# Kernel tuning notes

Hardware: AMD Instinct MI355X
Metric: run time of the kernel (lower is better)

The kernel has to match this reference:

```python
import jax, jax.numpy as jnp
import numpy as np

B, C, H, W = 8, 192, 56, 56
OUT, K = 192, 9
BN_EPS = 1e-5


def _l2_normalize(x, axis):
    # matches torch F.normalize: x / max(||x||, eps)
    n = jnp.sqrt(jnp.sum(x * x, axis=axis, keepdims=True))
    return x / jnp.maximum(n, 1e-12)


def _knn_idx(x_bnc, k):
    # dense pairwise squared distances, then k nearest (includes self)
    sq = jnp.sum(x_bnc * x_bnc, axis=-1, keepdims=True)            # (b,n,1)
    dist = sq - 2.0 * jnp.einsum('bnc,bmc->bnm', x_bnc, x_bnc) + jnp.swapaxes(sq, 1, 2)
    _, idx = jax.lax.top_k(-dist, k)                                # (b,n,k)
    return idx


def setup_inputs() -> dict:
    key = jax.random.key(0)
    k1, k2 = jax.random.split(key)
    fan_in = 2 * C
    return {
        'x': jax.random.normal(k1, (B, C, H, W), dtype=jnp.float32),
        'conv_w': jax.random.normal(k2, (OUT, 2 * C), dtype=jnp.float32) * np.sqrt(2.0 / fan_in),
        'conv_b': jnp.zeros((OUT,), dtype=jnp.float32),
        'bn_gamma': jnp.ones((OUT,), dtype=jnp.float32),
        'bn_beta': jnp.zeros((OUT,), dtype=jnp.float32),
    }


def reference(x, conv_w, conv_b, bn_gamma, bn_beta):
    b, c, h, w = x.shape
    n = h * w
    xf = x.reshape(b, c, n)                      # (b,c,n) node features
    xt = jnp.swapaxes(xf, 1, 2)                  # (b,n,c)

    # graph build on L2-normalized features (torch does this under no_grad)
    xn = _l2_normalize(xt, axis=-1)
    idx = _knn_idx(jax.lax.stop_gradient(xn), K)  # (b,n,K) neighbor ids

    # gather neighbors; center gather is identity (center_idx == arange)
    x_j = jnp.take_along_axis(xt[:, :, None, :], idx[..., None], axis=1)  # (b,n,K,c)
    x_i = xt[:, :, None, :]                                               # (b,n,1,c)
    feat = jnp.concatenate([jnp.broadcast_to(x_i, x_j.shape), x_j - x_i], axis=-1)  # (b,n,K,2c)

    # 1x1 conv == per-edge linear
    y = jnp.einsum('bnke,oe->bnko', feat, conv_w) + conv_b                # (b,n,K,out)

    # BatchNorm2d (training-mode batch stats over b,n,K per channel)
    mean = jnp.mean(y, axis=(0, 1, 2))
    var = jnp.var(y, axis=(0, 1, 2))
    y = (y - mean) * jax.lax.rsqrt(var + BN_EPS) * bn_gamma + bn_beta

    y = jax.nn.gelu(y, approximate=False)
    y = jnp.max(y, axis=2)                        # max over K neighbors -> (b,n,out)
    return jnp.transpose(y, (0, 2, 1)).reshape(b, -1, h, w)
```

## Files before the change

### kernel.cpp

```cpp
#include <hip/hip_runtime.h>
#include <hip/hip_bf16.h>
#include <math.h>

#define BB 8
#define CC 192
#define HH 56
#define WW 56
#define NPTS 3136
#define OUTC 192
#define KNN 9
#define NTILES 49
#define NCH 2
#define NT4 98
#define NBLK4 (NT4 * BB)

typedef __bf16 bf16x8 __attribute__((ext_vector_type(8)));
typedef float  f32x16 __attribute__((ext_vector_type(16)));
typedef int    i32x4  __attribute__((ext_vector_type(4)));

__device__ __forceinline__ unsigned short f2bf(float f) {
    unsigned u = __float_as_uint(f);
    u += 0x7fffu + ((u >> 16) & 1u);
    return (unsigned short)(u >> 16);
}
__device__ __forceinline__ float bf2f(unsigned short h) {
    return __uint_as_float(((unsigned)h) << 16);
}
__device__ __forceinline__ float gelu_f(float z) {
    return 0.5f * z * (1.0f + erff(z * 0.70710678118654752f));
}

__device__ __forceinline__ void ins12u32(unsigned (&t)[12], unsigned key) {
    if (key >= t[11]) return;
    t[11] = key;
#pragma unroll
    for (int q = 11; q > 0; --q) {
        const unsigned a = t[q-1], bq = t[q];
        const bool sw = bq < a;
        t[q-1] = sw ? bq : a;
        t[q]   = sw ? a : bq;
    }
}

__device__ __forceinline__ void ins12u(unsigned long long (&t)[12], unsigned long long key) {
    if (key >= t[11]) return;
    t[11] = key;
#pragma unroll
    for (int q = 11; q > 0; --q) {
        const unsigned long long a = t[q-1], bq = t[q];
        const bool sw = bq < a;
        t[q-1] = sw ? bq : a;
        t[q]   = sw ? a : bq;
    }
}

__device__ __forceinline__ void ins9f(float (&d)[9], int (&ix)[9], float nd, int ni) {
    if (!((nd < d[8]) || (nd == d[8] && ni < ix[8]))) return;
    d[8] = nd; ix[8] = ni;
#pragma unroll
    for (int q = 8; q > 0; --q) {
        if ((d[q] < d[q-1]) || (d[q] == d[q-1] && ix[q] < ix[q-1])) {
            float t = d[q]; d[q] = d[q-1]; d[q-1] = t;
            int t2 = ix[q]; ix[q] = ix[q-1]; ix[q-1] = t2;
        }
    }
}

__global__ __launch_bounds__(256) void k1_normalize(const float* __restrict__ x,
                                                    float* __restrict__ xn,
                                                    unsigned short* __restrict__ xh,
                                                    unsigned short* __restrict__ xl,
                                                    float* __restrict__ normv,
                                                    float* __restrict__ sqv) {
    const int b  = blockIdx.y;
    const int n0 = blockIdx.x * 64;
    __shared__ float tile[64 * 193];
    __shared__ float red[4][64];
    __shared__ float inv[64];
    const int tid = threadIdx.x;
    const int p   = tid & 63;
    const int cg  = tid >> 6;
    const float* xb = x + (size_t)b * CC * NPTS;

    float acc = 0.f;
#pragma unroll 4
    for (int t = 0; t < 48; ++t) {
        const int c = cg * 48 + t;
        const float v = xb[(size_t)c * NPTS + n0 + p];
        tile[p * 193 + c] = v;
        acc += v * v;
    }
    red[cg][p] = acc;
    __syncthreads();
    if (cg == 0) {
        const float s  = red[0][p] + red[1][p] + red[2][p] + red[3][p];
        float nc = sqrtf(s);
        nc = fmaxf(nc, 1e-12f);
        normv[b * NPTS + n0 + p] = nc;
        const float iv = 1.0f / nc;
        inv[p] = iv;
        sqv[b * NPTS + n0 + p] = s * iv * iv;
    }
    __syncthreads();
    const size_t base = ((size_t)b * NPTS + n0) * CC;
    float* dst = xn + base;
    for (int q = tid; q < 64 * CC / 4; q += 256) {
        const int f   = q * 4;
        const int row = f / CC;
        const int c   = f - row * CC;
        const float iv = inv[row];
        float4 v;
        v.x = tile[row * 193 + c + 0] * iv;
        v.y = tile[row * 193 + c + 1] * iv;
        v.z = tile[row * 193 + c + 2] * iv;
        v.w = tile[row * 193 + c + 3] * iv;
        *(float4*)&dst[f] = v;
        ushort4 hv, lv;
        hv.x = f2bf(v.x); lv.x = f2bf(v.x - bf2f(hv.x));
        hv.y = f2bf(v.y); lv.y = f2bf(v.y - bf2f(hv.y));
        hv.z = f2bf(v.z); lv.z = f2bf(v.z - bf2f(hv.z));
        hv.w = f2bf(v.w); lv.w = f2bf(v.w - bf2f(hv.w));
        *(ushort4*)&xh[base + f] = hv;
        *(ushort4*)&xl[base + f] = lv;
    }
}

__global__ __launch_bounds__(256, 3) void k2_knn(const unsigned short* __restrict__ xh,
                                                 const unsigned short* __restrict__ xl,
                                                 unsigned long long* __restrict__ pd) {
    const int b     = blockIdx.x;
    const int chunk = blockIdx.y;
    const int r0    = blockIdx.z * 64;
    const int t0    = chunk ? 25 : 0;
    const int t1    = chunk ? 49 : 25;

    __shared__ __align__(16) char smem[51200];
    unsigned short* Cs  = (unsigned short*)smem;
    unsigned short* Rk1 = (unsigned short*)(smem + 25600);
    unsigned long long* cdu = (unsigned long long*)smem;

    const int tid  = threadIdx.x;
    const int w    = tid >> 6;
    const int lane = tid & 63;
    const int wc   = w & 1;
    const int wr   = w >> 1;
    const int l31  = lane & 31;
    const int lhi  = lane >> 5;
    const int koffe = lhi * 8;
    const int myrow = wc * 32 + l31;

    const int spnt = tid >> 2;
    const int sj   = tid & 3;

    const size_t rbase = ((size_t)b * NPTS + (r0 + myrow)) * CC;
    bf16x8 Rh0[6], Rl0[6];
#pragma unroll
    for (int c = 0; c < 6; ++c) {
        Rh0[c] = *(const bf16x8*)(const void*)(xh + rbase + c * 16 + koffe);
        Rl0[c] = *(const bf16x8*)(const void*)(xl + rbase + c * 16 + koffe);
    }

    {
        const size_t pb = ((size_t)b * NPTS + r0 + spnt) * CC + 96;
#pragma unroll
        for (int rep = 0; rep < 3; ++rep) {
            const int j = sj + rep * 4;
            *(uint4*)(void*)&Rk1[spnt * 200 + j * 8] =
                *(const uint4*)(const void*)(xh + pb + j * 8);
        }
#pragma unroll
        for (int rep = 0; rep < 3; ++rep) {
            const int j = sj + rep * 4;
            *(uint4*)(void*)&Rk1[spnt * 200 + 96 + j * 8] =
                *(const uint4*)(const void*)(xl + pb + j * 8);
        }
    }

    unsigned t12[12];
#pragma unroll
    for (int q = 0; q < 12; ++q) t12[q] = 0xFFFFFFFFu;

    const int cfb = (wr * 32 + l31) * 200 + koffe;
    const int rlb = myrow * 200 + koffe;

    for (int ct = t0; ct < t1; ++ct) {
        const int c0 = ct * 64;
        __syncthreads();
        {
            const size_t pb = ((size_t)b * NPTS + c0 + spnt) * CC;
#pragma unroll
            for (int rep = 0; rep < 6; ++rep) {
                const int j = sj + rep * 4;
                *(uint4*)(void*)&Cs[spnt * 200 + j * 8] =
                    *(const uint4*)(const void*)(xh + pb + j * 8);
            }
        }
        __syncthreads();

        f32x16 acc;
#pragma unroll
        for (int r = 0; r < 16; ++r) acc[r] = 0.f;

#pragma unroll
        for (int c = 0; c < 6; ++c) {
            const bf16x8 cf = *(const bf16x8*)(const void*)&Cs[cfb + c * 16];
            acc = __builtin_amdgcn_mfma_f32_32x32x16_bf16(cf, Rh0[c], acc, 0, 0, 0);
            acc = __builtin_amdgcn_mfma_f32_32x32x16_bf16(cf, Rl0[c], acc, 0, 0, 0);
        }
#pragma unroll
        for (int c = 0; c < 6; ++c) {
            const bf16x8 cf = *(const bf16x8*)(const void*)&Cs[cfb + (6 + c) * 16];
            const i32x4 th = *(const volatile i32x4*)(const volatile void*)&Rk1[rlb + c * 16];
            const i32x4 tl = *(const volatile i32x4*)(const volatile void*)&Rk1[rlb + 96 + c * 16];
            acc = __builtin_amdgcn_mfma_f32_32x32x16_bf16(cf, __builtin_bit_cast(bf16x8, th), acc, 0, 0, 0);
            acc = __builtin_amdgcn_mfma_f32_32x32x16_bf16(cf, __builtin_bit_cast(bf16x8, tl), acc, 0, 0, 0);
        }
        __syncthreads();
        {
            const size_t pb = ((size_t)b * NPTS + c0 + spnt) * CC;
#pragma unroll
            for (int rep = 0; rep < 6; ++rep) {
                const int j = sj + rep * 4;
                *(uint4*)(void*)&Cs[spnt * 200 + j * 8] =
                    *(const uint4*)(const void*)(xl + pb + j * 8);
            }
        }
        __syncthreads();
#pragma unroll
        for (int c = 0; c < 6; ++c) {
            const bf16x8 cl = *(const bf16x8*)(const void*)&Cs[cfb + c * 16];
            acc = __builtin_amdgcn_mfma_f32_32x32x16_bf16(cl, Rh0[c], acc, 0, 0, 0);
        }
#pragma unroll
        for (int c = 0; c < 6; ++c) {
            const bf16x8 cl = *(const bf16x8*)(const void*)&Cs[cfb + (6 + c) * 16];
            const i32x4 th = *(const volatile i32x4*)(const volatile void*)&Rk1[rlb + c * 16];
            acc = __builtin_amdgcn_mfma_f32_32x32x16_bf16(cl, __builtin_bit_cast(bf16x8, th), acc, 0, 0, 0);
        }

        const unsigned tbase = (unsigned)((ct - t0) << 4);
#pragma unroll
        for (int reg = 0; reg < 16; ++reg) {
            const float d = fmaxf(1.0f - acc[reg], 0.0f);
            const unsigned key = (__float_as_uint(d) & 0xFFFFFE00u) | (tbase | (unsigned)reg);
            ins12u32(t12, key);
        }
    }

    __syncthreads();
#pragma unroll
    for (int q = 0; q < 12; ++q) {
        const unsigned key = t12[q];
        const int tag = (int)(key & 511u);
        const int reg = tag & 15;
        const int col = (t0 + (tag >> 4)) * 64 + wr * 32 + ((reg & 3) + 8 * (reg >> 2) + 4 * lhi);
        cdu[(((wr * 2 + lhi) * 64) + myrow) * 12 + q] = ((unsigned long long)key << 32) | (unsigned)col;
    }
    __syncthreads();
    if (tid < 64) {
        unsigned long long t[12];
#pragma unroll
        for (int q = 0; q < 12; ++q) t[q] = cdu[tid * 12 + q];
        for (int s = 1; s < 4; ++s)
#pragma unroll
            for (int q = 0; q < 12; ++q) ins12u(t, cdu[(s * 64 + tid) * 12 + q]);
        const size_t gbase = ((size_t)b * NPTS + r0 + tid) * (NCH * 12) + chunk * 12;
#pragma unroll
        for (int q = 0; q < 12; ++q) pd[gbase + q] = t[q];
    }
}

__global__ __launch_bounds__(128) void k2b_merge(const float* __restrict__ xn,
                                                 const float* __restrict__ sqv,
                                                 const unsigned long long* __restrict__ pd,
                                                 int* __restrict__ idxout) {
    const int b  = blockIdx.x;
    const int r0 = blockIdx.y * 32;
    __shared__ __align__(16) float xr_s[32][196];
    __shared__ int   ci[32][12];
    __shared__ float dd[32][13];
    __shared__ int   need[32];
    const int tid = threadIdx.x;
    const float* xb = xn + (size_t)b * NPTS * CC;

    for (int q = tid; q < 32 * 48; q += 128) {
        const int row = q / 48, c4 = q - row * 48;
        *(float4*)&xr_s[row][c4 * 4] = *(const float4*)&xb[(size_t)(r0 + row) * CC + c4 * 4];
    }
    if (tid < 32) {
        const size_t base = ((size_t)b * NPTS + r0 + tid) * (NCH * 12);
        unsigned long long t[12];
#pragma unroll
        for (int q = 0; q < 12; ++q) t[q] = pd[base + q];
        for (int s = 1; s < NCH; ++s)
#pragma unroll
            for (int q = 0; q < 12; ++q) ins12u(t, pd[base + s * 12 + q]);
#pragma unroll
        for (int q = 0; q < 12; ++q) ci[tid][q] = (int)(t[q] & 0xFFFFFFFFull);
        const float d9  = __uint_as_float((unsigned)(t[8] >> 32) & 0xFFFFFE00u);
        const float d10 = __uint_as_float((unsigned)(t[9] >> 32) & 0xFFFFFE00u);
        need[tid] = (d10 - d9) < 3e-4f ? 1 : 0;
    }
    __syncthreads();
    {
        const int p = tid >> 2;
        const int s = tid & 3;
        if (need[p]) {
            const float sqn = sqv[(size_t)b * NPTS + r0 + p];
#pragma unroll
            for (int t3 = 0; t3 < 3; ++t3) {
                const int cs2 = s + t3 * 4;
                const int m   = ci[p][cs2];
                const float* xm = xb + (size_t)m * CC;
                float4 a4 = make_float4(0.f, 0.f, 0.f, 0.f);
#pragma unroll 8
                for (int c4 = 0; c4 < 48; ++c4) {
                    const float4 xv = *(const float4*)&xm[c4 * 4];
                    const float4 rv = *(const float4*)&xr_s[p][c4 * 4];
                    a4.x += rv.x * xv.x;
                    a4.y += rv.y * xv.y;
                    a4.z += rv.z * xv.z;
                    a4.w += rv.w * xv.w;
                }
                const float dot = (a4.x + a4.y) + (a4.z + a4.w);
                dd[p][cs2] = sqn + sqv[(size_t)b * NPTS + m] - 2.0f * dot;
            }
        }
    }
    __syncthreads();
    if (tid < 32) {
        int* orow = &idxout[((size_t)b * NPTS + r0 + tid) * KNN];
        if (need[tid]) {
            float fd[9]; int fi[9];
#pragma unroll
            for (int q = 0; q < 9; ++q) { fd[q] = 3.4e38f; fi[q] = 0x7fffffff; }
#pragma unroll
            for (int cs2 = 0; cs2 < 12; ++cs2)
                ins9f(fd, fi, dd[tid][cs2], ci[tid][cs2]);
#pragma unroll
            for (int q = 0; q < 9; ++q) orow[q] = fi[q];
        } else {
#pragma unroll
            for (int q = 0; q < 9; ++q) orow[q] = ci[tid][q];
        }
    }
}

__global__ __launch_bounds__(256) void k3a_wcat(const float* __restrict__ cw,
                                               unsigned short* __restrict__ wh,
                                               unsigned short* __restrict__ wl) {
    const int i = blockIdx.x * 256 + threadIdx.x;
    if (i < 2 * OUTC * CC) {
        const int r = i / CC, c = i - r * CC;
        float val;
        if (r < OUTC) val = cw[r * (2 * CC) + c] - cw[r * (2 * CC) + CC + c];
        else          val = cw[(r - OUTC) * (2 * CC) + CC + c];
        const unsigned short h = f2bf(val);
        wh[i] = h;
        wl[i] = f2bf(val - bf2f(h));
    }
}

__global__ __launch_bounds__(256) void k3_mfma(const unsigned short* __restrict__ xh,
                                               const unsigned short* __restrict__ xl,
                                               const unsigned short* __restrict__ wh,
                                               const unsigned short* __restrict__ wl,
                                               const float* __restrict__ normv,
                                               const float* __restrict__ conv_b,
                                               float* __restrict__ uv) {
    const int m0 = blockIdx.x * 64;
    const int o0 = blockIdx.y * 64;
    const int tid  = threadIdx.x;
    const int w    = tid >> 6;
    const int lane = tid & 63;
    const int wr   = w >> 1;
    const int wc   = w & 1;
    const int l31  = lane & 31;
    const int lhi  = lane >> 5;
    const int koffe = lhi * 8;

    const size_t abase = (size_t)(m0 + wr * 32 + l31) * CC;
    bf16x8 Ah[12], Al[12];
#pragma unroll
    for (int c = 0; c < 12; ++c) {
        Ah[c] = *(const bf16x8*)(const void*)(xh + abase + c * 16 + koffe);
        Al[c] = *(const bf16x8*)(const void*)(xl + abase + c * 16 + koffe);
    }
    const int o = o0 + wc * 32 + l31;
    const unsigned short* whr = wh + (size_t)o * CC;
    const unsigned short* wlr = wl + (size_t)o * CC;

    f32x16 acc;
#pragma unroll
    for (int r = 0; r < 16; ++r) acc[r] = 0.f;
#pragma unroll
    for (int c = 0; c < 12; ++c) {
        const bf16x8 bh = *(const bf16x8*)(const void*)(whr + c * 16 + koffe);
        const bf16x8 bl = *(const bf16x8*)(const void*)(wlr + c * 16 + koffe);
        acc = __builtin_amdgcn_mfma_f32_32x32x16_bf16(Ah[c], bh, acc, 0, 0, 0);
        acc = __builtin_amdgcn_mfma_f32_32x32x16_bf16(Al[c], bh, acc, 0, 0, 0);
        acc = __builtin_amdgcn_mfma_f32_32x32x16_bf16(Ah[c], bl, acc, 0, 0, 0);
    }
    const float bias = (o < OUTC) ? conv_b[o] : 0.0f;
#pragma unroll
    for (int reg = 0; reg < 16; ++reg) {
        const int m = m0 + wr * 32 + (reg & 3) + 8 * (reg >> 2) + 4 * lhi;
        uv[(size_t)m * (2 * OUTC) + o] = acc[reg] * normv[m] + bias;
    }
}

__global__ __launch_bounds__(256) void k4_fused(const float* __restrict__ uv,
                                                const int* __restrict__ idxb,
                                                float* __restrict__ amax,
                                                float* __restrict__ amin,
                                                float* __restrict__ partials) {
    const int flat = blockIdx.x;
    const int b    = flat & 7;
    const int tile = flat >> 3;
    const int tid  = threadIdx.x;
    const int p    = tid >> 3;
    const int g    = tid & 7;
    const int n    = tile * 32 + p;
    const size_t base = (size_t)b * NPTS;
    __shared__ float red[256 * 25];

    float sv[24], sv2[24], vmx[24], vmn[24];
#pragma unroll
    for (int c = 0; c < 24; ++c) { sv[c] = 0.f; sv2[c] = 0.f; vmx[c] = -3.4e38f; vmn[c] = 3.4e38f; }

    const int* ix = &idxb[(base + n) * KNN];
#pragma unroll
    for (int k = 0; k < KNN; ++k) {
        const int m = ix[k];
        const float* vr = &uv[(base + m) * (2 * OUTC) + OUTC + g * 24];
#pragma unroll
        for (int c4 = 0; c4 < 6; ++c4) {
            const float4 v = *(const float4*)&vr[c4 * 4];
            const int c = c4 * 4;
            sv[c+0] += v.x; sv2[c+0] += v.x*v.x; vmx[c+0] = fmaxf(vmx[c+0], v.x); vmn[c+0] = fminf(vmn[c+0], v.x);
            sv[c+1] += v.y; sv2[c+1] += v.y*v.y; vmx[c+1] = fmaxf(vmx[c+1], v.y); vmn[c+1] = fminf(vmn[c+1], v.y);
            sv[c+2] += v.z; sv2[c+2] += v.z*v.z; vmx[c+2] = fmaxf(vmx[c+2], v.z); vmn[c+2] = fminf(vmn[c+2], v.z);
            sv[c+3] += v.w; sv2[c+3] += v.w*v.w; vmx[c+3] = fmaxf(vmx[c+3], v.w); vmn[c+3] = fminf(vmn[c+3], v.w);
        }
    }
    const float* ur = &uv[(base + n) * (2 * OUTC) + g * 24];
    float S[24], Q[24];
    float* am = &amax[(base + n) * OUTC + g * 24];
    float* an = &amin[(base + n) * OUTC + g * 24];
#pragma unroll
    for (int c4 = 0; c4 < 6; ++c4) {
        const float4 u4 = *(const float4*)&ur[c4 * 4];
        const int c = c4 * 4;
        float4 mx, mn;
        mx.x = u4.x + vmx[c+0]; mn.x = u4.x + vmn[c+0];
        mx.y = u4.y + vmx[c+1]; mn.y = u4.y + vmn[c+1];
        mx.z = u4.z + vmx[c+2]; mn.z = u4.z + vmn[c+2];
        mx.w = u4.w + vmx[c+3]; mn.w = u4.w + vmn[c+3];
        *(float4*)&am[c4 * 4] = mx;
        *(float4*)&an[c4 * 4] = mn;
        S[c+0] = 9.f*u4.x + sv[c+0];  Q[c+0] = u4.x*(9.f*u4.x + 2.f*sv[c+0]) + sv2[c+0];
        S[c+1] = 9.f*u4.y + sv[c+1];  Q[c+1] = u4.y*(9.f*u4.y + 2.f*sv[c+1]) + sv2[c+1];
        S[c+2] = 9.f*u4.z + sv[c+2];  Q[c+2] = u4.z*(9.f*u4.z + 2.f*sv[c+2]) + sv2[c+2];
        S[c+3] = 9.f*u4.w + sv[c+3];  Q[c+3] = u4.w*(9.f*u4.w + 2.f*sv[c+3]) + sv2[c+3];
    }
#pragma unroll
    for (int c = 0; c < 24; ++c) red[tid * 25 + c] = S[c];
    __syncthreads();
    float accS = 0.f;
    if (tid < OUTC) {
        const int go = tid / 24, co = tid - go * 24;
        for (int pp = 0; pp < 32; ++pp) accS += red[(pp * 8 + go) * 25 + co];
    }
    __syncthreads();
#pragma unroll
    for (int c = 0; c < 24; ++c) red[tid * 25 + c] = Q[c];
    __syncthreads();
    if (tid < OUTC) {
        const int go = tid / 24, co = tid - go * 24;
        float accQ = 0.f;
        for (int pp = 0; pp < 32; ++pp) accQ += red[(pp * 8 + go) * 25 + co];
        partials[(size_t)flat * (2 * OUTC) + tid]        = accS;
        partials[(size_t)flat * (2 * OUTC) + OUTC + tid] = accQ;
    }
}

__global__ __launch_bounds__(256) void k4b_finalize(const float* __restrict__ partials,
                                                    const float* __restrict__ gamma,
                                                    const float* __restrict__ beta,
                                                    float* __restrict__ scsh) {
    const int o   = blockIdx.x;
    const int tid = threadIdx.x;
    __shared__ float sS[256], sQ[256];
    float S = 0.f, Q = 0.f;
    for (int blk = tid; blk < NBLK4; blk += 256) {
        S += partials[(size_t)blk * (2 * OUTC) + o];
        Q += partials[(size_t)blk * (2 * OUTC) + OUTC + o];
    }
    sS[tid] = S; sQ[tid] = Q;
    __syncthreads();
    for (int s = 128; s > 0; s >>= 1) {
        if (tid < s) { sS[tid] += sS[tid + s]; sQ[tid] += sQ[tid + s]; }
        __syncthreads();
    }
    if (tid == 0) {
        const float cnt  = (float)BB * (float)NPTS * (float)KNN;
        const float mean = sS[0] / cnt;
        float var = fmaxf(sQ[0] / cnt - mean * mean, 0.0f);
        const float scale = gamma[o] * rsqrtf(var + 1e-5f);
        scsh[o]        = scale;
        scsh[OUTC + o] = beta[o] - mean * scale;
    }
}

__global__ __launch_bounds__(256) void k5_out(const float* __restrict__ amax,
                                              const float* __restrict__ amin,
                                              const float* __restrict__ scsh,
                                              float* __restrict__ out) {
    const int b  = blockIdx.y;
    const int n0 = blockIdx.x * 64;
    __shared__ float zb[64 * 193];
    __shared__ float ssc[OUTC];
    __shared__ float ssh[OUTC];
    const int tid = threadIdx.x;
    for (int q = tid; q < OUTC; q += 256) {
        ssc[q] = scsh[q];
        ssh[q] = scsh[OUTC + q];
    }
    __syncthreads();
    const int p  = tid >> 2;
    const int og = tid & 3;
    const int n  = n0 + p;
    const size_t rb = ((size_t)b * NPTS + n) * OUTC + og * 48;
#pragma unroll
    for (int t4 = 0; t4 < 12; ++t4) {
        const float4 ax = *(const float4*)&amax[rb + t4 * 4];
        const float4 an = *(const float4*)&amin[rb + t4 * 4];
        const int ob = og * 48 + t4 * 4;
        float z1, z2;
        z1 = ax.x * ssc[ob+0] + ssh[ob+0]; z2 = an.x * ssc[ob+0] + ssh[ob+0];
        zb[p * 193 + ob + 0] = fmaxf(gelu_f(z1), gelu_f(z2));
        z1 = ax.y * ssc[ob+1] + ssh[ob+1]; z2 = an.y * ssc[ob+1] + ssh[ob+1];
        zb[p * 193 + ob + 1] = fmaxf(gelu_f(z1), gelu_f(z2));
        z1 = ax.z * ssc[ob+2] + ssh[ob+2]; z2 = an.z * ssc[ob+2] + ssh[ob+2];
        zb[p * 193 + ob + 2] = fmaxf(gelu_f(z1), gelu_f(z2));
        z1 = ax.w * ssc[ob+3] + ssh[ob+3]; z2 = an.w * ssc[ob+3] + ssh[ob+3];
        zb[p * 193 + ob + 3] = fmaxf(gelu_f(z1), gelu_f(z2));
    }
    __syncthreads();
    float* ob2 = out + (size_t)b * OUTC * NPTS;
    for (int q = tid; q < 64 * OUTC; q += 256) {
        const int o  = q >> 6;
        const int pp = q & 63;
        ob2[(size_t)o * NPTS + n0 + pp] = zb[pp * 193 + o];
    }
}

extern "C" void kernel_launch(void* const* d_in, const int* in_sizes, int n_in,
                              void* d_out, int out_size, void* d_ws, size_t ws_size,
                              hipStream_t stream) {
    const float* x        = (const float*)d_in[0];
    const float* conv_w   = (const float*)d_in[1];
    const float* conv_b   = (const float*)d_in[2];
    const float* bn_gamma = (const float*)d_in[3];
    const float* bn_beta  = (const float*)d_in[4];
    float* out = (float*)d_out;

    float* ws = (float*)d_ws;
    const size_t SZ_XN = (size_t)BB * NPTS * CC;
    const size_t SZ_NV = (size_t)BB * NPTS;
    const size_t SZ_A  = (size_t)BB * NPTS * OUTC;

    int*   idxb        = (int*)ws;
    unsigned short* wh = (unsigned short*)(idxb + (size_t)BB * NPTS * KNN);
    unsigned short* wl = wh + (size_t)(2 * OUTC) * CC;
    float* uv       = (float*)(wl + (size_t)(2 * OUTC) * CC);
    float* partials = uv + (size_t)BB * NPTS * (2 * OUTC);
    float* scsh     = partials + (size_t)NBLK4 * (2 * OUTC);
    float* normv    = scsh + 2 * OUTC;
    float* sqv      = normv + SZ_NV;
    float* xn       = sqv + SZ_NV;
    unsigned short* xh = (unsigned short*)(xn + SZ_XN);
    unsigned short* xl = xh + SZ_XN;
    unsigned long long* pd = (unsigned long long*)uv;
    float* amax = xn;
    float* amin = xn + SZ_A;

    k1_normalize<<<dim3(NTILES, BB), 256, 0, stream>>>(x, xn, xh, xl, normv, sqv);
    k2_knn<<<dim3(BB, NCH, NTILES), 256, 0, stream>>>(xh, xl, pd);
    k2b_merge<<<dim3(BB, NT4), 128, 0, stream>>>(xn, sqv, pd, idxb);
    k3a_wcat<<<(2 * OUTC * CC + 255) / 256, 256, 0, stream>>>(conv_w, wh, wl);
    k3_mfma<<<dim3(BB * NPTS / 64, (2 * OUTC) / 64), 256, 0, stream>>>(xh, xl, wh, wl, normv, conv_b, uv);
    k4_fused<<<NBLK4, 256, 0, stream>>>(uv, idxb, amax, amin, partials);
    k4b_finalize<<<OUTC, 256, 0, stream>>>(partials, bn_gamma, bn_beta, scsh);
    k5_out<<<dim3(NTILES, BB), 256, 0, stream>>>(amax, amin, scsh, out);
}
```

Measured before the change: 388.6 us.

## Merge KNN and conv GEMM into one launch to run them concurrently

Combines the KNN distance/top-k kernel and the per-point conv GEMM kernel into a single launch, with each block choosing a role from its block index. The two independent stages can then share the GPU, letting the GEMM blocks fill compute units left idle by the KNN tail. Because uv is now written while pd is still live, pd moves to a separate workspace region after xl. The shared kernel takes on KNN's launch bounds and 51KB of shared memory, which can limit occupancy for the GEMM blocks.

```diff
diff --git a/kernel.cpp b/kernel.cpp
--- a/kernel.cpp
+++ b/kernel.cpp
@@ -13,6 +13,8 @@
 #define NCH 2
 #define NT4 98
 #define NBLK4 (NT4 * BB)
+#define K2BLKS (BB * NCH * NTILES)
+#define K3BLKS ((BB * NPTS / 64) * 6)
 
 typedef __bf16 bf16x8 __attribute__((ext_vector_type(8)));
 typedef float  f32x16 __attribute__((ext_vector_type(16)));
@@ -125,148 +127,193 @@
     }
 }
 
-__global__ __launch_bounds__(256, 3) void k2_knn(const unsigned short* __restrict__ xh,
-                                                 const unsigned short* __restrict__ xl,
-                                                 unsigned long long* __restrict__ pd) {
-    const int b     = blockIdx.x;
-    const int chunk = blockIdx.y;
-    const int r0    = blockIdx.z * 64;
-    const int t0    = chunk ? 25 : 0;
-    const int t1    = chunk ? 49 : 25;
-
+__global__ __launch_bounds__(256, 3) void k23_mega(const unsigned short* __restrict__ xh,
+                                                   const unsigned short* __restrict__ xl,
+                                                   unsigned long long* __restrict__ pd,
+                                                   const unsigned short* __restrict__ wh,
+                                                   const unsigned short* __restrict__ wl,
+                                                   const float* __restrict__ normv,
+                                                   const float* __restrict__ conv_b,
+                                                   float* __restrict__ uv) {
     __shared__ __align__(16) char smem[51200];
-    unsigned short* Cs  = (unsigned short*)smem;
-    unsigned short* Rk1 = (unsigned short*)(smem + 25600);
-    unsigned long long* cdu = (unsigned long long*)smem;
-
-    const int tid  = threadIdx.x;
+    const int bid = blockIdx.x;
+    const int tid = threadIdx.x;
     const int w    = tid >> 6;
     const int lane = tid & 63;
-    const int wc   = w & 1;
-    const int wr   = w >> 1;
     const int l31  = lane & 31;
     const int lhi  = lane >> 5;
     const int koffe = lhi * 8;
-    const int myrow = wc * 32 + l31;
-
-    const int spnt = tid >> 2;
-    const int sj   = tid & 3;
-
-    const size_t rbase = ((size_t)b * NPTS + (r0 + myrow)) * CC;
-    bf16x8 Rh0[6], Rl0[6];
-#pragma unroll
-    for (int c = 0; c < 6; ++c) {
-        Rh0[c] = *(const bf16x8*)(const void*)(xh + rbase + c * 16 + koffe);
-        Rl0[c] = *(const bf16x8*)(const void*)(xl + rbase + c * 16 + koffe);
-    }
-
-    {
-        const size_t pb = ((size_t)b * NPTS + r0 + spnt) * CC + 96;
-#pragma unroll
-        for (int rep = 0; rep < 3; ++rep) {
-            const int j = sj + rep * 4;
-            *(uint4*)(void*)&Rk1[spnt * 200 + j * 8] =
-                *(const uint4*)(const void*)(xh + pb + j * 8);
-        }
-#pragma unroll
-        for (int rep = 0; rep < 3; ++rep) {
-            const int j = sj + rep * 4;
-            *(uint4*)(void*)&Rk1[spnt * 200 + 96 + j * 8] =
-                *(const uint4*)(const void*)(xl + pb + j * 8);
-        }
-    }
-
-    unsigned t12[12];
-#pragma unroll
-    for (int q = 0; q < 12; ++q) t12[q] = 0xFFFFFFFFu;
-
-    const int cfb = (wr * 32 + l31) * 200 + koffe;
-    const int rlb = myrow * 200 + koffe;
-
-    for (int ct = t0; ct < t1; ++ct) {
-        const int c0 = ct * 64;
+
+    if (bid < K2BLKS) {
+        const int b     = bid & 7;
+        const int chunk = (bid >> 3) & 1;
+        const int r0    = (bid >> 4) * 64;
+        const int t0    = chunk ? 25 : 0;
+        const int t1    = chunk ? 49 : 25;
+
+        unsigned short* Cs  = (unsigned short*)smem;
+        unsigned short* Rk1 = (unsigned short*)(smem + 25600);
+        unsigned long long* cdu = (unsigned long long*)smem;
+
+        const int wc   = w & 1;
+        const int wr   = w >> 1;
+        const int myrow = wc * 32 + l31;
+        const int spnt = tid >> 2;
+        const int sj   = tid & 3;
+
+        const size_t rbase = ((size_t)b * NPTS + (r0 + myrow)) * CC;
+        bf16x8 Rh0[6], Rl0[6];
+#pragma unroll
+        for (int c = 0; c < 6; ++c) {
+            Rh0[c] = *(const bf16x8*)(const void*)(xh + rbase + c * 16 + koffe);
+            Rl0[c] = *(const bf16x8*)(const void*)(xl + rbase + c * 16 + koffe);
+        }
+
+        {
+            const size_t pb = ((size_t)b * NPTS + r0 + spnt) * CC + 96;
+#pragma unroll
+            for (int rep = 0; rep < 3; ++rep) {
+                const int j = sj + rep * 4;
+                *(uint4*)(void*)&Rk1[spnt * 200 + j * 8] =
+                    *(const uint4*)(const void*)(xh + pb + j * 8);
+            }
+#pragma unroll
+            for (int rep = 0; rep < 3; ++rep) {
+                const int j = sj + rep * 4;
+                *(uint4*)(void*)&Rk1[spnt * 200 + 96 + j * 8] =
+                    *(const uint4*)(const void*)(xl + pb + j * 8);
+            }
+        }
+
+        unsigned t12[12];
+#pragma unroll
+        for (int q = 0; q < 12; ++q) t12[q] = 0xFFFFFFFFu;
+
+        const int cfb = (wr * 32 + l31) * 200 + koffe;
+        const int rlb = myrow * 200 + koffe;
+
+        for (int ct = t0; ct < t1; ++ct) {
+            const int c0 = ct * 64;
+            __syncthreads();
+            {
+                const size_t pb = ((size_t)b * NPTS + c0 + spnt) * CC;
+#pragma unroll
+                for (int rep = 0; rep < 6; ++rep) {
+                    const int j = sj + rep * 4;
+                    *(uint4*)(void*)&Cs[spnt * 200 + j * 8] =
+                        *(const uint4*)(const void*)(xh + pb + j * 8);
+                }
+            }
+            __syncthreads();
+
+            f32x16 acc;
+#pragma unroll
+            for (int r = 0; r < 16; ++r) acc[r] = 0.f;
+
+#pragma unroll
+            for (int c = 0; c < 6; ++c) {
+                const bf16x8 cf = *(const bf16x8*)(const void*)&Cs[cfb + c * 16];
+                acc = __builtin_amdgcn_mfma_f32_32x32x16_bf16(cf, Rh0[c], acc, 0, 0, 0);
+                acc = __builtin_amdgcn_mfma_f32_32x32x16_bf16(cf, Rl0[c], acc, 0, 0, 0);
+            }
+#pragma unroll
+            for (int c = 0; c < 6; ++c) {
+                const bf16x8 cf = *(const bf16x8*)(const void*)&Cs[cfb + (6 + c) * 16];
+                const i32x4 th = *(const volatile i32x4*)(const volatile void*)&Rk1[rlb + c * 16];
+                const i32x4 tl = *(const volatile i32x4*)(const volatile void*)&Rk1[rlb + 96 + c * 16];
+                acc = __builtin_amdgcn_mfma_f32_32x32x16_bf16(cf, __builtin_bit_cast(bf16x8, th), acc, 0, 0, 0);
+                acc = __builtin_amdgcn_mfma_f32_32x32x16_bf16(cf, __builtin_bit_cast(bf16x8, tl), acc, 0, 0, 0);
+            }
+            __syncthreads();
+            {
+                const size_t pb = ((size_t)b * NPTS + c0 + spnt) * CC;
+#pragma unroll
+                for (int rep = 0; rep < 6; ++rep) {
+                    const int j = sj + rep * 4;
+                    *(uint4*)(void*)&Cs[spnt * 200 + j * 8] =
+                        *(const uint4*)(const void*)(xl + pb + j * 8);
+                }
+            }
+            __syncthreads();
+#pragma unroll
+            for (int c = 0; c < 6; ++c) {
+                const bf16x8 cl = *(const bf16x8*)(const void*)&Cs[cfb + c * 16];
+                acc = __builtin_amdgcn_mfma_f32_32x32x16_bf16(cl, Rh0[c], acc, 0, 0, 0);
+            }
+#pragma unroll
+            for (int c = 0; c < 6; ++c) {
+                const bf16x8 cl = *(const bf16x8*)(const void*)&Cs[cfb + (6 + c) * 16];
+                const i32x4 th = *(const volatile i32x4*)(const volatile void*)&Rk1[rlb + c * 16];
+                acc = __builtin_amdgcn_mfma_f32_32x32x16_bf16(cl, __builtin_bit_cast(bf16x8, th), acc, 0, 0, 0);
+            }
+
+            const unsigned tbase = (unsigned)((ct - t0) << 4);
+#pragma unroll
+            for (int reg = 0; reg < 16; ++reg) {
+                const float d = fmaxf(1.0f - acc[reg], 0.0f);
+                const unsigned key = (__float_as_uint(d) & 0xFFFFFE00u) | (tbase | (unsigned)reg);
+                ins12u32(t12, key);
+            }
+        }
+
         __syncthreads();
-        {
-            const size_t pb = ((size_t)b * NPTS + c0 + spnt) * CC;
-#pragma unroll
-            for (int rep = 0; rep < 6; ++rep) {
-                const int j = sj + rep * 4;
-                *(uint4*)(void*)&Cs[spnt * 200 + j * 8] =
-                    *(const uint4*)(const void*)(xh + pb + j * 8);
-            }
+#pragma unroll
+        for (int q = 0; q < 12; ++q) {
+            const unsigned key = t12[q];
+            const int tag = (int)(key & 511u);
+            const int reg = tag & 15;
+            const int col = (t0 + (tag >> 4)) * 64 + wr * 32 + ((reg & 3) + 8 * (reg >> 2) + 4 * lhi);
+            cdu[(((wr * 2 + lhi) * 64) + myrow) * 12 + q] = ((unsigned long long)key << 32) | (unsigned)col;
         }
         __syncthreads();
+        if (tid < 64) {
+            unsigned long long t[12];
+#pragma unroll
+            for (int q = 0; q < 12; ++q) t[q] = cdu[tid * 12 + q];
+            for (int s = 1; s < 4; ++s)
+#pragma unroll
+                for (int q = 0; q < 12; ++q) ins12u(t, cdu[(s * 64 + tid) * 12 + q]);
+            const size_t gbase = ((size_t)b * NPTS + r0 + tid) * (NCH * 12) + chunk * 12;
+#pragma unroll
+            for (int q = 0; q < 12; ++q) pd[gbase + q] = t[q];
+        }
+    } else {
+        const int id2 = bid - K2BLKS;
+        const int ot  = id2 % 6;
+        const int mt  = id2 / 6;
+        const int m0  = mt * 64;
+        const int o0  = ot * 64;
+        const int wr  = w >> 1;
+        const int wc  = w & 1;
+
+        const size_t abase = (size_t)(m0 + wr * 32 + l31) * CC;
+        bf16x8 Ah[12], Al[12];
+#pragma unroll
+        for (int c = 0; c < 12; ++c) {
+            Ah[c] = *(const bf16x8*)(const void*)(xh + abase + c * 16 + koffe);
+            Al[c] = *(const bf16x8*)(const void*)(xl + abase + c * 16 + koffe);
+        }
+        const int o = o0 + wc * 32 + l31;
+        const unsigned short* whr = wh + (size_t)o * CC;
+        const unsigned short* wlr = wl + (size_t)o * CC;
 
         f32x16 acc;
 #pragma unroll
         for (int r = 0; r < 16; ++r) acc[r] = 0.f;
-
-#pragma unroll
-        for (int c = 0; c < 6; ++c) {
-            const bf16x8 cf = *(const bf16x8*)(const void*)&Cs[cfb + c * 16];
-            acc = __builtin_amdgcn_mfma_f32_32x32x16_bf16(cf, Rh0[c], acc, 0, 0, 0);
-            acc = __builtin_amdgcn_mfma_f32_32x32x16_bf16(cf, Rl0[c], acc, 0, 0, 0);
-        }
-#pragma unroll
-        for (int c = 0; c < 6; ++c) {
-            const bf16x8 cf = *(const bf16x8*)(const void*)&Cs[cfb + (6 + c) * 16];
-            const i32x4 th = *(const volatile i32x4*)(const volatile void*)&Rk1[rlb + c * 16];
-            const i32x4 tl = *(const volatile i32x4*)(const volatile void*)&Rk1[rlb + 96 + c * 16];
-            acc = __builtin_amdgcn_mfma_f32_32x32x16_bf16(cf, __builtin_bit_cast(bf16x8, th), acc, 0, 0, 0);
-            acc = __builtin_amdgcn_mfma_f32_32x32x16_bf16(cf, __builtin_bit_cast(bf16x8, tl), acc, 0, 0, 0);
-        }
-        __syncthreads();
-        {
-            const size_t pb = ((size_t)b * NPTS + c0 + spnt) * CC;
-#pragma unroll
-            for (int rep = 0; rep < 6; ++rep) {
-                const int j = sj + rep * 4;
-                *(uint4*)(void*)&Cs[spnt * 200 + j * 8] =
-                    *(const uint4*)(const void*)(xl + pb + j * 8);
-            }
-        }
-        __syncthreads();
-#pragma unroll
-        for (int c = 0; c < 6; ++c) {
-            const bf16x8 cl = *(const bf16x8*)(const void*)&Cs[cfb + c * 16];
-            acc = __builtin_amdgcn_mfma_f32_32x32x16_bf16(cl, Rh0[c], acc, 0, 0, 0);
-        }
-#pragma unroll
-        for (int c = 0; c < 6; ++c) {
-            const bf16x8 cl = *(const bf16x8*)(const void*)&Cs[cfb + (6 + c) * 16];
-            const i32x4 th = *(const volatile i32x4*)(const volatile void*)&Rk1[rlb + c * 16];
-            acc = __builtin_amdgcn_mfma_f32_32x32x16_bf16(cl, __builtin_bit_cast(bf16x8, th), acc, 0, 0, 0);
-        }
-
-        const unsigned tbase = (unsigned)((ct - t0) << 4);
+#pragma unroll
+        for (int c = 0; c < 12; ++c) {
+            const bf16x8 bh = *(const bf16x8*)(const void*)(whr + c * 16 + koffe);
+            const bf16x8 bl = *(const bf16x8*)(const void*)(wlr + c * 16 + koffe);
+            acc = __builtin_amdgcn_mfma_f32_32x32x16_bf16(Ah[c], bh, acc, 0, 0, 0);
+            acc = __builtin_amdgcn_mfma_f32_32x32x16_bf16(Al[c], bh, acc, 0, 0, 0);
+            acc = __builtin_amdgcn_mfma_f32_32x32x16_bf16(Ah[c], bl, acc, 0, 0, 0);
+        }
+        const float bias = (o < OUTC) ? conv_b[o] : 0.0f;
 #pragma unroll
         for (int reg = 0; reg < 16; ++reg) {
-            const float d = fmaxf(1.0f - acc[reg], 0.0f);
-            const unsigned key = (__float_as_uint(d) & 0xFFFFFE00u) | (tbase | (unsigned)reg);
-            ins12u32(t12, key);
-        }
-    }
-
-    __syncthreads();
-#pragma unroll
-    for (int q = 0; q < 12; ++q) {
-        const unsigned key = t12[q];
-        const int tag = (int)(key & 511u);
-        const int reg = tag & 15;
-        const int col = (t0 + (tag >> 4)) * 64 + wr * 32 + ((reg & 3) + 8 * (reg >> 2) + 4 * lhi);
-        cdu[(((wr * 2 + lhi) * 64) + myrow) * 12 + q] = ((unsigned long long)key << 32) | (unsigned)col;
-    }
-    __syncthreads();
-    if (tid < 64) {
-        unsigned long long t[12];
-#pragma unroll
-        for (int q = 0; q < 12; ++q) t[q] = cdu[tid * 12 + q];
-        for (int s = 1; s < 4; ++s)
-#pragma unroll
-            for (int q = 0; q < 12; ++q) ins12u(t, cdu[(s * 64 + tid) * 12 + q]);
-        const size_t gbase = ((size_t)b * NPTS + r0 + tid) * (NCH * 12) + chunk * 12;
-#pragma unroll
-        for (int q = 0; q < 12; ++q) pd[gbase + q] = t[q];
+            const int m = m0 + wr * 32 + (reg & 3) + 8 * (reg >> 2) + 4 * lhi;
+            uv[(size_t)m * (2 * OUTC) + o] = acc[reg] * normv[m] + bias;
+        }
     }
 }
 
@@ -361,54 +408,6 @@
     }
 }
 
-__global__ __launch_bounds__(256) void k3_mfma(const unsigned short* __restrict__ xh,
-                                               const unsigned short* __restrict__ xl,
-                                               const unsigned short* __restrict__ wh,
-                                               const unsigned short* __restrict__ wl,
-                                               const float* __restrict__ normv,
-                                               const float* __restrict__ conv_b,
-                                               float* __restrict__ uv) {
-    const int m0 = blockIdx.x * 64;
-    const int o0 = blockIdx.y * 64;
-    const int tid  = threadIdx.x;
-    const int w    = tid >> 6;
-    const int lane = tid & 63;
-    const int wr   = w >> 1;
-    const int wc   = w & 1;
-    const int l31  = lane & 31;
-    const int lhi  = lane >> 5;
-    const int koffe = lhi * 8;
-
-    const size_t abase = (size_t)(m0 + wr * 32 + l31) * CC;
-    bf16x8 Ah[12], Al[12];
-#pragma unroll
-    for (int c = 0; c < 12; ++c) {
-        Ah[c] = *(const bf16x8*)(const void*)(xh + abase + c * 16 + koffe);
-        Al[c] = *(const bf16x8*)(const void*)(xl + abase + c * 16 + koffe);
-    }
-    const int o = o0 + wc * 32 + l31;
-    const unsigned short* whr = wh + (size_t)o * CC;
-    const unsigned short* wlr = wl + (size_t)o * CC;
-
-    f32x16 acc;
-#pragma unroll
-    for (int r = 0; r < 16; ++r) acc[r] = 0.f;
-#pragma unroll
-    for (int c = 0; c < 12; ++c) {
-        const bf16x8 bh = *(const bf16x8*)(const void*)(whr + c * 16 + koffe);
-        const bf16x8 bl = *(const bf16x8*)(const void*)(wlr + c * 16 + koffe);
-        acc = __builtin_amdgcn_mfma_f32_32x32x16_bf16(Ah[c], bh, acc, 0, 0, 0);
-        acc = __builtin_amdgcn_mfma_f32_32x32x16_bf16(Al[c], bh, acc, 0, 0, 0);
-        acc = __builtin_amdgcn_mfma_f32_32x32x16_bf16(Ah[c], bl, acc, 0, 0, 0);
-    }
-    const float bias = (o < OUTC) ? conv_b[o] : 0.0f;
-#pragma unroll
-    for (int reg = 0; reg < 16; ++reg) {
-        const int m = m0 + wr * 32 + (reg & 3) + 8 * (reg >> 2) + 4 * lhi;
-        uv[(size_t)m * (2 * OUTC) + o] = acc[reg] * normv[m] + bias;
-    }
-}
-
 __global__ __launch_bounds__(256) void k4_fused(const float* __restrict__ uv,
                                                 const int* __restrict__ idxb,
                                                 float* __restrict__ amax,
@@ -581,15 +580,14 @@
     float* xn       = sqv + SZ_NV;
     unsigned short* xh = (unsigned short*)(xn + SZ_XN);
     unsigned short* xl = xh + SZ_XN;
-    unsigned long long* pd = (unsigned long long*)uv;
+    unsigned long long* pd = (unsigned long long*)(xl + SZ_XN);
     float* amax = xn;
     float* amin = xn + SZ_A;
 
     k1_normalize<<<dim3(NTILES, BB), 256, 0, stream>>>(x, xn, xh, xl, normv, sqv);
-    k2_knn<<<dim3(BB, NCH, NTILES), 256, 0, stream>>>(xh, xl, pd);
+    k3a_wcat<<<(2 * OUTC * CC + 255) / 256, 256, 0, stream>>>(conv_w, wh, wl);
+    k23_mega<<<K2BLKS + K3BLKS, 256, 0, stream>>>(xh, xl, pd, wh, wl, normv, conv_b, uv);
     k2b_merge<<<dim3(BB, NT4), 128, 0, stream>>>(xn, sqv, pd, idxb);
-    k3a_wcat<<<(2 * OUTC * CC + 255) / 256, 256, 0, stream>>>(conv_w, wh, wl);
-    k3_mfma<<<dim3(BB * NPTS / 64, (2 * OUTC) / 64), 256, 0, stream>>>(xh, xl, wh, wl, normv, conv_b, uv);
     k4_fused<<<NBLK4, 256, 0, stream>>>(uv, idxb, amax, amin, partials);
     k4b_finalize<<<OUTC, 256, 0, stream>>>(partials, bn_gamma, bn_beta, scsh);
     k5_out<<<dim3(NTILES, BB), 256, 0, stream>>>(amax, amin, scsh, out);
```

New measurement: 349.7 us (median of 2 runs). 1.11x faster.
